# Kernel optimization log

Measured on AMD Instinct MI355X. Metric: run time of the kernel, lower is better.

The kernel has to match this reference:

```python
import jax, jax.numpy as jnp
import numpy as np

D_MODEL = 768
NUM_HEADS = 12
D_K = D_MODEL // NUM_HEADS


def setup_inputs() -> dict:
    key = jax.random.key(0)
    ks = jax.random.split(key, 5)
    B, S = 2, 2048
    scale = 1.0 / np.sqrt(D_MODEL)
    return {
        "x": jax.random.normal(ks[0], (B, S, D_MODEL), dtype=jnp.float32),
        "q_proj_weight": jax.random.normal(ks[1], (D_MODEL, D_MODEL), dtype=jnp.float32) * scale,
        "k_proj_weight": jax.random.normal(ks[2], (D_MODEL, D_MODEL), dtype=jnp.float32) * scale,
        "v_proj_weight": jax.random.normal(ks[3], (D_MODEL, D_MODEL), dtype=jnp.float32) * scale,
        "o_proj_weight": jax.random.normal(ks[4], (D_MODEL, D_MODEL), dtype=jnp.float32) * scale,
    }


def reference(x, q_proj_weight, k_proj_weight, v_proj_weight, o_proj_weight):
    B, S, _ = x.shape
    H, dk = NUM_HEADS, D_K
    # projections: weight is [d_out, d_in], applied as x @ W^T
    Q = jnp.einsum("bsd,ed->bse", x, q_proj_weight).reshape(B, S, H, dk)
    K = jnp.einsum("bsd,ed->bse", x, k_proj_weight).reshape(B, S, H, dk)
    V = jnp.einsum("bsd,ed->bse", x, v_proj_weight).reshape(B, S, H, dk)
    # scores [b, h, q, k]
    scores = jnp.einsum("bqhd,bkhd->bhqk", Q, K) / jnp.sqrt(jnp.float32(dk))
    causal = jnp.tril(jnp.ones((S, S), dtype=bool))
    scores = jnp.where(causal, scores, -jnp.inf)
    attn = jax.nn.softmax(scores, axis=-1)
    out = jnp.einsum("bhqk,bkhd->bqhd", attn, V).reshape(B, S, H * dk)
    return jnp.einsum("bsd,ed->bse", out, o_proj_weight)
```

## Files before the change

### kernel.cpp

```cpp
#include <hip/hip_runtime.h>
#include <hip/hip_bf16.h>
#include <stdint.h>

typedef __hip_bfloat16 bf16;
typedef __attribute__((ext_vector_type(8))) short short8;
typedef __attribute__((ext_vector_type(4))) float f32x4;
typedef __attribute__((ext_vector_type(16))) float f32x16;

#define MFMA16(A, B, C) __builtin_amdgcn_mfma_f32_16x16x32_bf16(A, B, C, 0, 0, 0)
#define MFMA32(A, B, C) __builtin_amdgcn_mfma_f32_32x32x16_bf16(A, B, C, 0, 0, 0)

#define SB 2
#define SS 2048
#define SD 768
#define SH 12
#define SM (SB*SS)
#define BHSD (SB*SH*SS*64)
#define QSCALE 0.18033688011112042f

__device__ __forceinline__ void gload_lds16(const bf16* g, bf16* l) {
    __builtin_amdgcn_global_load_lds(
        (const __attribute__((address_space(1))) void*)(g),
        (__attribute__((address_space(3))) void*)(l),
        16, 0, 0);
}

__device__ __forceinline__ int cvtpk(float a, float b) {
    int r;
    asm("v_cvt_pk_bf16_f32 %0, %1, %2" : "=v"(r) : "v"(a), "v"(b));
    return r;
}
__device__ __forceinline__ void plswap(int& a, int& b) {
    asm("v_permlane32_swap_b32 %0, %1" : "+v"(a), "+v"(b));
}

__global__ void cvt_all(const float4* __restrict__ x,  const float4* __restrict__ w0,
                        const float4* __restrict__ w1, const float4* __restrict__ w2,
                        const float4* __restrict__ w3,
                        uint64_t* __restrict__ xb, uint64_t* __restrict__ wqkv,
                        uint64_t* __restrict__ wob) {
    int bid = blockIdx.x;
    const float4* s; uint64_t* d; int base;
    if (bid < 3072) { s = x; d = xb; base = bid << 8; }
    else {
        int t = bid - 3072, seg = t / 576, li = t - seg * 576;
        s = (seg == 0) ? w0 : (seg == 1) ? w1 : (seg == 2) ? w2 : w3;
        d = (seg < 3) ? (wqkv + seg * 147456) : wob;
        base = li << 8;
    }
    int i = base + threadIdx.x;
    float4 v = s[i];
    union { bf16 h[4]; uint64_t u; } p;
    p.h[0] = __float2bfloat16(v.x);
    p.h[1] = __float2bfloat16(v.y);
    p.h[2] = __float2bfloat16(v.z);
    p.h[3] = __float2bfloat16(v.w);
    d[i] = p.u;
}

template<int EPI>
__global__ __launch_bounds__(256) void gemm_bt(const bf16* __restrict__ A,
                                               const bf16* __restrict__ Bw,
                                               void* __restrict__ Out,
                                               int K) {
    __shared__ bf16 lA[128 * 64];
    __shared__ bf16 lB[128 * 64];
    const int tid  = threadIdx.x;
    const int lane = tid & 63;
    const int wid  = tid >> 6;
    const int wr = wid >> 1, wc = wid & 1;
    const int m0 = blockIdx.y * 128, n0 = blockIdx.x * 128;
    const int g = lane >> 4, l15 = lane & 15;
    const int srow = lane >> 3, slot = lane & 7;

    f32x4 acc[4][4] = {};

    for (int kt = 0; kt < K; kt += 64) {
        __syncthreads();
        #pragma unroll
        for (int p = 0; p < 4; ++p) {
            int c = wid * 4 + p;
            int row = c * 8 + srow;
            int colsw = (slot ^ (row & 7)) * 8;
            gload_lds16(A  + (m0 + row) * K + kt + colsw, &lA[c * 512]);
            gload_lds16(Bw + (n0 + row) * K + kt + colsw, &lB[c * 512]);
        }
        __syncthreads();
        #pragma unroll
        for (int ks = 0; ks < 2; ++ks) {
            short8 af[4], bfv[4];
            #pragma unroll
            for (int m = 0; m < 4; ++m) {
                int row = wr * 64 + m * 16 + l15;
                int idx = row * 64 + (((ks * 4 + g) ^ (row & 7)) * 8);
                af[m] = *reinterpret_cast<const short8*>(&lA[idx]);
            }
            #pragma unroll
            for (int n = 0; n < 4; ++n) {
                int row = wc * 64 + n * 16 + l15;
                int idx = row * 64 + (((ks * 4 + g) ^ (row & 7)) * 8);
                bfv[n] = *reinterpret_cast<const short8*>(&lB[idx]);
            }
            #pragma unroll
            for (int m = 0; m < 4; ++m)
                #pragma unroll
                for (int n = 0; n < 4; ++n)
                    acc[m][n] = MFMA16(af[m], bfv[n], acc[m][n]);
        }
    }

    #pragma unroll
    for (int m = 0; m < 4; ++m) {
        #pragma unroll
        for (int n = 0; n < 4; ++n) {
            int col = n0 + wc * 64 + n * 16 + l15;
            #pragma unroll
            for (int r = 0; r < 4; ++r) {
                int row = m0 + wr * 64 + m * 16 + g * 4 + r;
                float v = acc[m][n][r];
                if constexpr (EPI == 0) {
                    int which = (col >= 1536) ? 2 : (col >= 768 ? 1 : 0);
                    int e = col - which * 768;
                    int h = e >> 6, d = e & 63;
                    int b = row >> 11, s = row & 2047;
                    int bh = b * SH + h;
                    bf16* dst = (bf16*)Out;
                    int idx;
                    if (which == 2) idx = 2 * BHSD + (bh * 64 + d) * SS + s;
                    else            idx = which * BHSD + (bh * SS + s) * 64 + d;
                    if (which == 0) v *= QSCALE;
                    dst[idx] = __float2bfloat16(v);
                } else {
                    ((float*)Out)[row * SD + col] = v;
                }
            }
        }
    }
}

__global__ __launch_bounds__(64) void attn_kernel(const bf16* __restrict__ Qb,
                                                  const bf16* __restrict__ Kb,
                                                  const bf16* __restrict__ Vtb,
                                                  bf16* __restrict__ AO) {
    __shared__ float bc[32];

    const int orig = blockIdx.x;
    const int xcd = orig & 7, li = orig >> 3;
    const int bh = xcd * 3 + (li >> 6);
    const int p = li & 63;
    const int j = (p < 32) ? (63 - p) : (p - 32);

    const int b = bh / SH, h = bh - b * SH;
    const int lane = threadIdx.x;
    const int l31 = lane & 31, hi = lane >> 5;

    const bf16* Qh = Qb + bh * SS * 64;
    const bf16* Kh = Kb + bh * SS * 64;
    const bf16* Vh = Vtb + bh * 64 * SS;

    const int qself = j * 32 + l31;
    short8 qf[4];
    #pragma unroll
    for (int ks = 0; ks < 4; ++ks)
        qf[ks] = *reinterpret_cast<const short8*>(Qh + qself * 64 + ks * 16 + hi * 8);

    f32x16 oacc[2];
    #pragma unroll
    for (int n = 0; n < 2; ++n)
        #pragma unroll
        for (int r = 0; r < 16; ++r) oacc[n][r] = 0.f;
    float lrow = 0.f;

    const bf16* kbase = Kh + l31 * 64 + hi * 8;
    const bf16* vbase = Vh + l31 * SS + hi * 8;

#define LDG(pp) (*reinterpret_cast<const short8*>(pp))

#define LOADSET2(K00, K01, K02, K03, K10, K11, K12, K13,                     \
                 V00, V01, V02, V03, V10, V11, V12, V13, P) do {             \
    const bf16* kp0_ = kbase + (2 * (P)) * 2048;                             \
    K00 = LDG(kp0_);        K01 = LDG(kp0_ + 16);                            \
    K02 = LDG(kp0_ + 32);   K03 = LDG(kp0_ + 48);                            \
    K10 = LDG(kp0_ + 2048); K11 = LDG(kp0_ + 2064);                          \
    K12 = LDG(kp0_ + 2080); K13 = LDG(kp0_ + 2096);                          \
    const bf16* vp0_ = vbase + (2 * (P)) * 32;                               \
    V00 = LDG(vp0_);             V01 = LDG(vp0_ + 16);                       \
    V02 = LDG(vp0_ + 65536);     V03 = LDG(vp0_ + 65536 + 16);               \
    V10 = LDG(vp0_ + 32);        V11 = LDG(vp0_ + 48);                       \
    V12 = LDG(vp0_ + 65536 + 32);V13 = LDG(vp0_ + 65536 + 48);               \
} while (0)

#define TILE2_BODY(K00, K01, K02, K03, K10, K11, K12, K13,                   \
                   V00, V01, V02, V03, V10, V11, V12, V13, PT) do {          \
    const int T0_ = 2 * (PT), T1_ = T0_ + 1;                                 \
    f32x16 s0_, s1_;                                                         \
    _Pragma("unroll")                                                        \
    for (int r = 0; r < 16; ++r) { s0_[r] = 0.f; s1_[r] = 0.f; }             \
    __builtin_amdgcn_s_setprio(1);                                           \
    s0_ = MFMA32(K00, qf[0], s0_);  s1_ = MFMA32(K10, qf[0], s1_);           \
    s0_ = MFMA32(K01, qf[1], s0_);  s1_ = MFMA32(K11, qf[1], s1_);           \
    s0_ = MFMA32(K02, qf[2], s0_);  s1_ = MFMA32(K12, qf[2], s1_);           \
    s0_ = MFMA32(K03, qf[3], s0_);  s1_ = MFMA32(K13, qf[3], s1_);           \
    __builtin_amdgcn_s_setprio(0);                                           \
    if (T0_ == j) {                                                          \
        _Pragma("unroll")                                                    \
        for (int r = 0; r < 16; ++r) {                                       \
            int kvrow = (r & 3) + 8 * (r >> 2) + 4 * hi;                     \
            if (kvrow > l31) s0_[r] = -1e30f;                                \
        }                                                                    \
    }                                                                        \
    if (T1_ == j) {                                                          \
        _Pragma("unroll")                                                    \
        for (int r = 0; r < 16; ++r) {                                       \
            int kvrow = (r & 3) + 8 * (r >> 2) + 4 * hi;                     \
            if (kvrow > l31) s1_[r] = -1e30f;                                \
        }                                                                    \
    } else if (T1_ > j) {                                                    \
        _Pragma("unroll")                                                    \
        for (int r = 0; r < 16; ++r) s1_[r] = -1e30f;                        \
    }                                                                        \
         \
    _Pragma("unroll")                                                        \
    for (int r = 0; r < 16; ++r) {                                           \
        s0_[r] = exp2f(s0_[r]);                                              \
        s1_[r] = exp2f(s1_[r]);                                              \
    }                                                                        \
    float w0 = ((s0_[0] + s0_[1]) + (s0_[2] + s0_[3]))                       \
             + ((s0_[4] + s0_[5]) + (s0_[6] + s0_[7]));                      \
    float w1 = ((s0_[8] + s0_[9]) + (s0_[10] + s0_[11]))                     \
             + ((s0_[12] + s0_[13]) + (s0_[14] + s0_[15]));                  \
    float w2 = ((s1_[0] + s1_[1]) + (s1_[2] + s1_[3]))                       \
             + ((s1_[4] + s1_[5]) + (s1_[6] + s1_[7]));                      \
    float w3 = ((s1_[8] + s1_[9]) + (s1_[10] + s1_[11]))                     \
             + ((s1_[12] + s1_[13]) + (s1_[14] + s1_[15]));                  \
    lrow += (w0 + w1) + (w2 + w3);                                           \
    int a0 = cvtpk(s0_[0],  s0_[1]),  a1 = cvtpk(s0_[2],  s0_[3]);           \
    int b0 = cvtpk(s0_[4],  s0_[5]),  b1 = cvtpk(s0_[6],  s0_[7]);           \
    plswap(a0, b0); plswap(a1, b1);                                          \
    int a2 = cvtpk(s0_[8],  s0_[9]),  a3 = cvtpk(s0_[10], s0_[11]);          \
    int b2 = cvtpk(s0_[12], s0_[13]), b3 = cvtpk(s0_[14], s0_[15]);          \
    plswap(a2, b2); plswap(a3, b3);                                          \
    int c0 = cvtpk(s1_[0],  s1_[1]),  c1 = cvtpk(s1_[2],  s1_[3]);           \
    int d0 = cvtpk(s1_[4],  s1_[5]),  d1 = cvtpk(s1_[6],  s1_[7]);           \
    plswap(c0, d0); plswap(c1, d1);                                          \
    int c2 = cvtpk(s1_[8],  s1_[9]),  c3 = cvtpk(s1_[10], s1_[11]);          \
    int d2 = cvtpk(s1_[12], s1_[13]), d3 = cvtpk(s1_[14], s1_[15]);          \
    plswap(c2, d2); plswap(c3, d3);                                          \
    union { int wd[4]; short8 s8; } u0_, u1_, u2_, u3_;                      \
    u0_.wd[0] = a0; u0_.wd[1] = a1; u0_.wd[2] = b0; u0_.wd[3] = b1;          \
    u1_.wd[0] = a2; u1_.wd[1] = a3; u1_.wd[2] = b2; u1_.wd[3] = b3;          \
    u2_.wd[0] = c0; u2_.wd[1] = c1; u2_.wd[2] = d0; u2_.wd[3] = d1;          \
    u3_.wd[0] = c2; u3_.wd[1] = c3; u3_.wd[2] = d2; u3_.wd[3] = d3;          \
    __builtin_amdgcn_s_setprio(1);                                           \
    oacc[0] = MFMA32(u0_.s8, V00, oacc[0]);                                  \
    oacc[1] = MFMA32(u0_.s8, V02, oacc[1]);                                  \
    oacc[0] = MFMA32(u1_.s8, V01, oacc[0]);                                  \
    oacc[1] = MFMA32(u1_.s8, V03, oacc[1]);                                  \
    oacc[0] = MFMA32(u2_.s8, V10, oacc[0]);                                  \
    oacc[1] = MFMA32(u2_.s8, V12, oacc[1]);                                  \
    oacc[0] = MFMA32(u3_.s8, V11, oacc[0]);                                  \
    oacc[1] = MFMA32(u3_.s8, V13, oacc[1]);                                  \
    __builtin_amdgcn_s_setprio(0);                                           \
} while (0)

    short8 kA00, kA01, kA02, kA03, kA10, kA11, kA12, kA13;
    short8 vA00, vA01, vA02, vA03, vA10, vA11, vA12, vA13;
    short8 kB00, kB01, kB02, kB03, kB10, kB11, kB12, kB13;
    short8 vB00, vB01, vB02, vB03, vB10, vB11, vB12, vB13;

    const int jp = j >> 1;

    LOADSET2(kA00,kA01,kA02,kA03,kA10,kA11,kA12,kA13,
             vA00,vA01,vA02,vA03,vA10,vA11,vA12,vA13, 0);
    LOADSET2(kB00,kB01,kB02,kB03,kB10,kB11,kB12,kB13,
             vB00,vB01,vB02,vB03,vB10,vB11,vB12,vB13, 1);

    int pt = 0;
    for (;;) {
        TILE2_BODY(kA00,kA01,kA02,kA03,kA10,kA11,kA12,kA13,
                   vA00,vA01,vA02,vA03,vA10,vA11,vA12,vA13, pt);
        LOADSET2(kA00,kA01,kA02,kA03,kA10,kA11,kA12,kA13,
                 vA00,vA01,vA02,vA03,vA10,vA11,vA12,vA13, pt + 2);
        ++pt;
        if (pt > jp) break;
        TILE2_BODY(kB00,kB01,kB02,kB03,kB10,kB11,kB12,kB13,
                   vB00,vB01,vB02,vB03,vB10,vB11,vB12,vB13, pt);
        LOADSET2(kB00,kB01,kB02,kB03,kB10,kB11,kB12,kB13,
                 vB00,vB01,vB02,vB03,vB10,vB11,vB12,vB13, pt + 2);
        ++pt;
        if (pt > jp) break;
    }

    lrow += __shfl_xor(lrow, 32);
    if (lane < 32) bc[lane] = 1.0f / lrow;
    f32x4 sv0 = *reinterpret_cast<f32x4*>(&bc[ 0 + 4 * hi]);
    f32x4 sv1 = *reinterpret_cast<f32x4*>(&bc[ 8 + 4 * hi]);
    f32x4 sv2 = *reinterpret_cast<f32x4*>(&bc[16 + 4 * hi]);
    f32x4 sv3 = *reinterpret_cast<f32x4*>(&bc[24 + 4 * hi]);
    #pragma unroll
    for (int n = 0; n < 2; ++n) {
        #pragma unroll
        for (int r = 0; r < 16; ++r) {
            int q = (r & 3) + 8 * (r >> 2) + 4 * hi;
            float f_ = (r >> 2) == 0 ? sv0[r & 3] :
                       (r >> 2) == 1 ? sv1[r & 3] :
                       (r >> 2) == 2 ? sv2[r & 3] : sv3[r & 3];
            float v = oacc[n][r] * f_;
            AO[(b * SS + j * 32 + q) * SD + h * 64 + n * 32 + l31] = __float2bfloat16(v);
        }
    }
}

extern "C" void kernel_launch(void* const* d_in, const int* in_sizes, int n_in,
                              void* d_out, int out_size, void* d_ws, size_t ws_size,
                              hipStream_t stream) {
    const float* x  = (const float*)d_in[0];
    const float* wq = (const float*)d_in[1];
    const float* wk = (const float*)d_in[2];
    const float* wv = (const float*)d_in[3];
    const float* wo = (const float*)d_in[4];
    float* out = (float*)d_out;

    bf16* xb   = (bf16*)d_ws;
    bf16* wqkv = xb + SM * SD;
    bf16* wob  = wqkv + 3 * SD * SD;
    bf16* qkv  = wob + SD * SD;
    bf16* ao   = qkv + 3 * BHSD;

    cvt_all<<<3072 + 4 * 576, 256, 0, stream>>>(
        (const float4*)x, (const float4*)wq, (const float4*)wk,
        (const float4*)wv, (const float4*)wo,
        (uint64_t*)xb, (uint64_t*)wqkv, (uint64_t*)wob);

    gemm_bt<0><<<dim3(2304 / 128, SM / 128), 256, 0, stream>>>(xb, wqkv, (void*)qkv, SD);
    attn_kernel<<<1536, 64, 0, stream>>>(qkv, qkv + BHSD, qkv + 2 * BHSD, ao);
    gemm_bt<1><<<dim3(SD / 128, SM / 128), 256, 0, stream>>>(ao, wob, (void*)out, SD);
}
```

Baseline: 127.1 us.

## Split attention KV range across blocks with atomic fp32 accumulation and normalize pass

Splits each causal query tile's KV loop into chunks of up to 8 pair-tiles, with long tiles spread over up to 4 blocks. Each block atomically adds its unnormalized output and row sums into zeroed fp32 buffers. A new kernel then divides by the row sums and writes the bf16 attention output. The aim is better load balance and more parallelism across CUs. The cost is a large memset, many fp32 global atomics and an extra kernel launch with its own memory traffic.

```diff
diff --git a/kernel.cpp b/kernel.cpp
--- a/kernel.cpp
+++ b/kernel.cpp
@@ -141,16 +141,20 @@
 __global__ __launch_bounds__(64) void attn_kernel(const bf16* __restrict__ Qb,
                                                   const bf16* __restrict__ Kb,
                                                   const bf16* __restrict__ Vtb,
-                                                  bf16* __restrict__ AO) {
-    __shared__ float bc[32];
-
-    const int orig = blockIdx.x;
-    const int xcd = orig & 7, li = orig >> 3;
-    const int bh = xcd * 3 + (li >> 6);
-    const int p = li & 63;
-    const int j = (p < 32) ? (63 - p) : (p - 32);
-
-    const int b = bh / SH, h = bh - b * SH;
+                                                  float* __restrict__ Op,
+                                                  float* __restrict__ lp) {
+    const int bid = blockIdx.x;
+    const int xcd = bid & 7, li = bid >> 3;
+    const int g160 = li / 160;
+    const int bh = xcd * 3 + g160;
+    const int u = li - g160 * 160;
+
+    int j, ck;
+    if (u < 16)      { j = u;                 ck = 0; }
+    else if (u < 48) { int t = u - 16; j = 16 + (t >> 1); ck = t & 1; }
+    else if (u < 96) { int t = u - 48; int q3 = t / 3; j = 32 + q3; ck = t - 3 * q3; }
+    else             { int t = u - 96; j = 48 + (t >> 2); ck = t & 3; }
+
     const int lane = threadIdx.x;
     const int l31 = lane & 31, hi = lane >> 5;
 
@@ -219,7 +223,7 @@
         _Pragma("unroll")                                                    \
         for (int r = 0; r < 16; ++r) s1_[r] = -1e30f;                        \
     }                                                                        \
-         \
+           \
     _Pragma("unroll")                                                        \
     for (int r = 0; r < 16; ++r) {                                           \
         s0_[r] = exp2f(s0_[r]);                                              \
@@ -269,46 +273,52 @@
     short8 vB00, vB01, vB02, vB03, vB10, vB11, vB12, vB13;
 
     const int jp = j >> 1;
+    const int p0 = ck * 8;
+    const int pe = (jp < p0 + 7) ? jp : (p0 + 7);
 
     LOADSET2(kA00,kA01,kA02,kA03,kA10,kA11,kA12,kA13,
-             vA00,vA01,vA02,vA03,vA10,vA11,vA12,vA13, 0);
+             vA00,vA01,vA02,vA03,vA10,vA11,vA12,vA13, p0);
     LOADSET2(kB00,kB01,kB02,kB03,kB10,kB11,kB12,kB13,
-             vB00,vB01,vB02,vB03,vB10,vB11,vB12,vB13, 1);
-
-    int pt = 0;
+             vB00,vB01,vB02,vB03,vB10,vB11,vB12,vB13, p0 + 1);
+
+    int pt = p0;
     for (;;) {
         TILE2_BODY(kA00,kA01,kA02,kA03,kA10,kA11,kA12,kA13,
                    vA00,vA01,vA02,vA03,vA10,vA11,vA12,vA13, pt);
         LOADSET2(kA00,kA01,kA02,kA03,kA10,kA11,kA12,kA13,
                  vA00,vA01,vA02,vA03,vA10,vA11,vA12,vA13, pt + 2);
         ++pt;
-        if (pt > jp) break;
+        if (pt > pe) break;
         TILE2_BODY(kB00,kB01,kB02,kB03,kB10,kB11,kB12,kB13,
                    vB00,vB01,vB02,vB03,vB10,vB11,vB12,vB13, pt);
         LOADSET2(kB00,kB01,kB02,kB03,kB10,kB11,kB12,kB13,
                  vB00,vB01,vB02,vB03,vB10,vB11,vB12,vB13, pt + 2);
         ++pt;
-        if (pt > jp) break;
-    }
-
-    lrow += __shfl_xor(lrow, 32);
-    if (lane < 32) bc[lane] = 1.0f / lrow;
-    f32x4 sv0 = *reinterpret_cast<f32x4*>(&bc[ 0 + 4 * hi]);
-    f32x4 sv1 = *reinterpret_cast<f32x4*>(&bc[ 8 + 4 * hi]);
-    f32x4 sv2 = *reinterpret_cast<f32x4*>(&bc[16 + 4 * hi]);
-    f32x4 sv3 = *reinterpret_cast<f32x4*>(&bc[24 + 4 * hi]);
+        if (pt > pe) break;
+    }
+
+    const int qrow0 = bh * SS + j * 32;
+    atomicAdd(&lp[qrow0 + l31], lrow);
     #pragma unroll
     for (int n = 0; n < 2; ++n) {
         #pragma unroll
         for (int r = 0; r < 16; ++r) {
             int q = (r & 3) + 8 * (r >> 2) + 4 * hi;
-            float f_ = (r >> 2) == 0 ? sv0[r & 3] :
-                       (r >> 2) == 1 ? sv1[r & 3] :
-                       (r >> 2) == 2 ? sv2[r & 3] : sv3[r & 3];
-            float v = oacc[n][r] * f_;
-            AO[(b * SS + j * 32 + q) * SD + h * 64 + n * 32 + l31] = __float2bfloat16(v);
+            int d = n * 32 + l31;
+            atomicAdd(&Op[(qrow0 + q) * 64 + d], oacc[n][r]);
         }
     }
+}
+
+__global__ __launch_bounds__(256) void norm_kernel(const float* __restrict__ Op,
+                                                   const float* __restrict__ lp,
+                                                   bf16* __restrict__ AO) {
+    int idx = blockIdx.x * 256 + threadIdx.x;
+    int d = idx & 63, srow = idx >> 6;
+    int bh = srow >> 11, s = srow & 2047;
+    int b = bh / SH, h = bh - b * SH;
+    float v = Op[idx] / lp[srow];
+    AO[(b * SS + s) * SD + h * 64 + d] = __float2bfloat16(v);
 }
 
 extern "C" void kernel_launch(void* const* d_in, const int* in_sizes, int n_in,
@@ -325,7 +335,11 @@
     bf16* wqkv = xb + SM * SD;
     bf16* wob  = wqkv + 3 * SD * SD;
     bf16* qkv  = wob + SD * SD;
-    bf16* ao   = qkv + 3 * BHSD;
+    float* Op  = (float*)(qkv + 3 * BHSD);
+    float* lp  = Op + SB * SH * SS * 64 / 64 * 64;
+    bf16* ao   = xb;
+
+    hipMemsetAsync(Op, 0, (3145728 + SB * SH * SS) * sizeof(float), stream);
 
     cvt_all<<<3072 + 4 * 576, 256, 0, stream>>>(
         (const float4*)x, (const float4*)wq, (const float4*)wk,
@@ -333,6 +347,7 @@
         (uint64_t*)xb, (uint64_t*)wqkv, (uint64_t*)wob);
 
     gemm_bt<0><<<dim3(2304 / 128, SM / 128), 256, 0, stream>>>(xb, wqkv, (void*)qkv, SD);
-    attn_kernel<<<1536, 64, 0, stream>>>(qkv, qkv + BHSD, qkv + 2 * BHSD, ao);
+    attn_kernel<<<3840, 64, 0, stream>>>(qkv, qkv + BHSD, qkv + 2 * BHSD, Op, lp);
+    norm_kernel<<<3145728 / 256, 256, 0, stream>>>(Op, lp, ao);
     gemm_bt<1><<<dim3(SD / 128, SM / 128), 256, 0, stream>>>(ao, wob, (void*)out, SD);
 }
```

Result: slower. 145.4 us (+14.4%).
